# Optimization experiments

Measured on AMD Instinct MI355X. Metric: run time of the kernel, lower is better.

## Reference

```python
import jax, jax.numpy as jnp
import numpy as np


def batch_map_offsets(x, offsets):
    """Bilinear sampling of x at (pixel grid + offsets), coords clipped to borders.
    x: [B,H,W,C], offsets: [B,H,W,2] (dy, dx) in pixels. Returns [B,H,W,C]."""
    B, H, W, C = x.shape
    gy, gx = jnp.meshgrid(jnp.arange(H, dtype=x.dtype), jnp.arange(W, dtype=x.dtype), indexing='ij')
    cy = jnp.clip(gy[None] + offsets[..., 0], 0.0, H - 1)
    cx = jnp.clip(gx[None] + offsets[..., 1], 0.0, W - 1)
    y0 = jnp.floor(cy).astype(jnp.int32)
    x0 = jnp.floor(cx).astype(jnp.int32)
    y1 = jnp.clip(y0 + 1, 0, H - 1)
    x1 = jnp.clip(x0 + 1, 0, W - 1)
    wy = (cy - y0.astype(x.dtype))[..., None]
    wx = (cx - x0.astype(x.dtype))[..., None]
    b = jnp.arange(B)[:, None, None]
    g = lambda yi, xi: x[b, yi, xi]  # gather -> [B,H,W,C]
    top = g(y0, x0) * (1 - wx) + g(y0, x1) * wx
    bot = g(y1, x0) * (1 - wx) + g(y1, x1) * wx
    return top * (1 - wy) + bot * wy


def setup_inputs() -> dict:
    key = jax.random.key(0)
    k1, k2 = jax.random.split(key)
    B, H, W, C = 8, 256, 256, 64
    x = jax.random.normal(k1, (B, H, W, C), dtype=jnp.float32)
    reg = jax.random.normal(k2, (B, H, W, 4), dtype=jnp.float32)
    return {"x": x, "reg": reg, "frame": 8, "share": 1}


def reference(x, reg, frame, share):
    reg_in, reg_out = jnp.split(reg, 2, axis=3)
    x_reg = batch_map_offsets(x, reg_in)            # [B,H,W,C]
    B, H, W, C = x_reg.shape
    xr = x_reg.reshape(1, frame, H, W, C)
    x_max = jnp.max(xr, axis=1)                     # [1,H,W,C]
    x_mean = jnp.mean(xr, axis=1)                   # [1,H,W,C]
    xs = jnp.concatenate([x_max, x_mean], axis=3)   # [1,H,W,2C]
    # stack over frame then reshape back to batch (same shared features per frame)
    xs = jnp.broadcast_to(xs[:, None], (1, frame, H, W, 2 * C)).reshape(B, H, W, 2 * C)
    x_share_1 = batch_map_offsets(xs, reg_out)      # [B,H,W,2C]
    x_share_2 = jnp.concatenate([x, x], axis=3)     # [B,H,W,2C]
    return jnp.where(jnp.asarray(share) != 0, x_share_1, x_share_2)
```

## Files before the change

### kernel.cpp

```cpp
#include <hip/hip_runtime.h>


__global__ __launch_bounds__(256) void share_reduce_kernel(
    const float* __restrict__ x, const float* __restrict__ reg,
    float* __restrict__ xs)
{
    const int wid  = threadIdx.x >> 6;
    const int lane = threadIdx.x & 63;
    const int pix  = (blockIdx.x << 2) + wid;
    const int h = pix >> 8;
    const int w = pix & 255;

    float vmax = -INFINITY;
    float vsum = 0.f;

#pragma unroll
    for (int b = 0; b < 8; ++b) {
        const float* rp = reg + ((((b << 8) + h) << 8) + w) * 4;
        const float dy = rp[0];
        const float dx = rp[1];
        float cy = fminf(fmaxf((float)h + dy, 0.f), 255.f);
        float cx = fminf(fmaxf((float)w + dx, 0.f), 255.f);
        const float fy0 = floorf(cy);
        const float fx0 = floorf(cx);
        const int y0 = (int)fy0;
        const int x0 = (int)fx0;
        const int y1 = min(y0 + 1, 255);
        const int x1 = min(x0 + 1, 255);
        const float wy = cy - fy0;
        const float wx = cx - fx0;

        const float* xb = x + ((size_t)b << 22);
        const float v00 = xb[(((y0 << 8) + x0) << 6) + lane];
        const float v01 = xb[(((y0 << 8) + x1) << 6) + lane];
        const float v10 = xb[(((y1 << 8) + x0) << 6) + lane];
        const float v11 = xb[(((y1 << 8) + x1) << 6) + lane];

        const float top = v00 * (1.f - wx) + v01 * wx;
        const float bot = v10 * (1.f - wx) + v11 * wx;
        const float val = top * (1.f - wy) + bot * wy;

        vmax = fmaxf(vmax, val);
        vsum += val;
    }

    float* op = xs + ((size_t)pix << 7);
    op[lane]      = vmax;
    op[64 + lane] = vsum * 0.125f;
}

__global__ __launch_bounds__(256) void share_sample_kernel(
    const float* __restrict__ x, const float* __restrict__ reg,
    const float* __restrict__ xs, const int* __restrict__ share_p,
    float* __restrict__ out)
{
    const int wid  = threadIdx.x >> 6;
    const int lane = threadIdx.x & 63;
    const int pix  = (blockIdx.x << 2) + wid;
    const int hw = pix & 65535;
    const int h = hw >> 8;
    const int w = hw & 255;

    float* op = out + ((size_t)pix << 7);

    if (*share_p != 0) {
        const float* rp = reg + (size_t)pix * 4;
        const float dy = rp[2];
        const float dx = rp[3];
        float cy = fminf(fmaxf((float)h + dy, 0.f), 255.f);
        float cx = fminf(fmaxf((float)w + dx, 0.f), 255.f);
        const float fy0 = floorf(cy);
        const float fx0 = floorf(cx);
        const int y0 = (int)fy0;
        const int x0 = (int)fx0;
        const int y1 = min(y0 + 1, 255);
        const int x1 = min(x0 + 1, 255);
        const float wy = cy - fy0;
        const float wx = cx - fx0;

        const float2* r00 = (const float2*)(xs + ((size_t)(((y0 << 8) + x0)) << 7)) + lane;
        const float2* r01 = (const float2*)(xs + ((size_t)(((y0 << 8) + x1)) << 7)) + lane;
        const float2* r10 = (const float2*)(xs + ((size_t)(((y1 << 8) + x0)) << 7)) + lane;
        const float2* r11 = (const float2*)(xs + ((size_t)(((y1 << 8) + x1)) << 7)) + lane;
        const float2 v00 = *r00;
        const float2 v01 = *r01;
        const float2 v10 = *r10;
        const float2 v11 = *r11;

        float2 res;
        {
            const float top = v00.x * (1.f - wx) + v01.x * wx;
            const float bot = v10.x * (1.f - wx) + v11.x * wx;
            res.x = top * (1.f - wy) + bot * wy;
        }
        {
            const float top = v00.y * (1.f - wx) + v01.y * wx;
            const float bot = v10.y * (1.f - wx) + v11.y * wx;
            res.y = top * (1.f - wy) + bot * wy;
        }
        ((float2*)op)[lane] = res;
    } else {
        const float v = x[((size_t)pix << 6) + lane];
        op[lane]      = v;
        op[64 + lane] = v;
    }
}

extern "C" void kernel_launch(void* const* d_in, const int* in_sizes, int n_in,
                              void* d_out, int out_size, void* d_ws, size_t ws_size,
                              hipStream_t stream) {
    const float* x     = (const float*)d_in[0];
    const float* reg   = (const float*)d_in[1];
    const int*   share = (const int*)d_in[3];
    float* out = (float*)d_out;
    float* xs  = (float*)d_ws;

    share_reduce_kernel<<<65536 / 4, 256, 0, stream>>>(x, reg, xs);
    share_sample_kernel<<<524288 / 4, 256, 0, stream>>>(x, reg, xs, share, out);
}
```

Before: 471.1 us.

## Widen per-thread vector loads and swizzle block-to-pixel mapping in both kernels

Each wave now handles two pixels, with 32 lanes per pixel. The reduce kernel uses float2 loads and the sample kernel uses float4 loads and nontemporal float4 stores, so the grids shrink by half and by two. Block indices are interleaved so that adjacent hardware blocks work on spatially separated rows. The aim is fewer, wider memory instructions and less cache pollution from the large output write. The cost is different gather coalescing and a changed locality pattern from the swizzle.

```diff
diff --git a/kernel.cpp b/kernel.cpp
--- a/kernel.cpp
+++ b/kernel.cpp
@@ -1,26 +1,30 @@
 #include <hip/hip_runtime.h>
 
+
+typedef float f32x2 __attribute__((ext_vector_type(2)));
+typedef float f32x4 __attribute__((ext_vector_type(4)));
 
 __global__ __launch_bounds__(256) void share_reduce_kernel(
     const float* __restrict__ x, const float* __restrict__ reg,
     float* __restrict__ xs)
 {
-    const int wid  = threadIdx.x >> 6;
-    const int lane = threadIdx.x & 63;
-    const int pix  = (blockIdx.x << 2) + wid;
+    const int bid  = ((blockIdx.x & 7) << 10) + (blockIdx.x >> 3);
+    const int tid  = threadIdx.x;
+    const int half = (tid >> 5) & 1;
+    const int ln   = tid & 31;
+    const int pix  = (bid << 3) + ((tid >> 6) << 1) + half;
     const int h = pix >> 8;
     const int w = pix & 255;
+    const int c = ln << 1;
 
-    float vmax = -INFINITY;
-    float vsum = 0.f;
+    float m0 = -INFINITY, m1 = -INFINITY;
+    float s0 = 0.f, s1 = 0.f;
 
 #pragma unroll
     for (int b = 0; b < 8; ++b) {
-        const float* rp = reg + ((((b << 8) + h) << 8) + w) * 4;
-        const float dy = rp[0];
-        const float dx = rp[1];
-        float cy = fminf(fmaxf((float)h + dy, 0.f), 255.f);
-        float cx = fminf(fmaxf((float)w + dx, 0.f), 255.f);
+        const f32x2 r = *(const f32x2*)(reg + (size_t)((((b << 8) + h) << 8) + w) * 4);
+        float cy = fminf(fmaxf((float)h + r.x, 0.f), 255.f);
+        float cx = fminf(fmaxf((float)w + r.y, 0.f), 255.f);
         const float fy0 = floorf(cy);
         const float fx0 = floorf(cx);
         const int y0 = (int)fy0;
@@ -31,22 +35,29 @@
         const float wx = cx - fx0;
 
         const float* xb = x + ((size_t)b << 22);
-        const float v00 = xb[(((y0 << 8) + x0) << 6) + lane];
-        const float v01 = xb[(((y0 << 8) + x1) << 6) + lane];
-        const float v10 = xb[(((y1 << 8) + x0) << 6) + lane];
-        const float v11 = xb[(((y1 << 8) + x1) << 6) + lane];
+        const f32x2 v00 = *(const f32x2*)(xb + ((((y0 << 8) + x0) << 6) + c));
+        const f32x2 v01 = *(const f32x2*)(xb + ((((y0 << 8) + x1) << 6) + c));
+        const f32x2 v10 = *(const f32x2*)(xb + ((((y1 << 8) + x0) << 6) + c));
+        const f32x2 v11 = *(const f32x2*)(xb + ((((y1 << 8) + x1) << 6) + c));
 
-        const float top = v00 * (1.f - wx) + v01 * wx;
-        const float bot = v10 * (1.f - wx) + v11 * wx;
-        const float val = top * (1.f - wy) + bot * wy;
+        const float t0 = v00.x * (1.f - wx) + v01.x * wx;
+        const float t1 = v00.y * (1.f - wx) + v01.y * wx;
+        const float u0 = v10.x * (1.f - wx) + v11.x * wx;
+        const float u1 = v10.y * (1.f - wx) + v11.y * wx;
+        const float val0 = t0 * (1.f - wy) + u0 * wy;
+        const float val1 = t1 * (1.f - wy) + u1 * wy;
 
-        vmax = fmaxf(vmax, val);
-        vsum += val;
+        m0 = fmaxf(m0, val0);
+        m1 = fmaxf(m1, val1);
+        s0 += val0;
+        s1 += val1;
     }
 
     float* op = xs + ((size_t)pix << 7);
-    op[lane]      = vmax;
-    op[64 + lane] = vsum * 0.125f;
+    f32x2 vmax; vmax.x = m0; vmax.y = m1;
+    f32x2 vmean; vmean.x = s0 * 0.125f; vmean.y = s1 * 0.125f;
+    *(f32x2*)(op + c)      = vmax;
+    *(f32x2*)(op + 64 + c) = vmean;
 }
 
 __global__ __launch_bounds__(256) void share_sample_kernel(
@@ -54,21 +65,22 @@
     const float* __restrict__ xs, const int* __restrict__ share_p,
     float* __restrict__ out)
 {
-    const int wid  = threadIdx.x >> 6;
-    const int lane = threadIdx.x & 63;
-    const int pix  = (blockIdx.x << 2) + wid;
+    const int bid  = ((blockIdx.x & 7) << 13) + (blockIdx.x >> 3);
+    const int tid  = threadIdx.x;
+    const int half = (tid >> 5) & 1;
+    const int ln   = tid & 31;
+    const int pix  = (bid << 3) + ((tid >> 6) << 1) + half;
     const int hw = pix & 65535;
     const int h = hw >> 8;
     const int w = hw & 255;
+    const int c = ln << 2;
 
     float* op = out + ((size_t)pix << 7);
 
     if (*share_p != 0) {
-        const float* rp = reg + (size_t)pix * 4;
-        const float dy = rp[2];
-        const float dx = rp[3];
-        float cy = fminf(fmaxf((float)h + dy, 0.f), 255.f);
-        float cx = fminf(fmaxf((float)w + dx, 0.f), 255.f);
+        const f32x4 r = *(const f32x4*)(reg + (size_t)pix * 4);
+        float cy = fminf(fmaxf((float)h + r.z, 0.f), 255.f);
+        float cx = fminf(fmaxf((float)w + r.w, 0.f), 255.f);
         const float fy0 = floorf(cy);
         const float fx0 = floorf(cx);
         const int y0 = (int)fy0;
@@ -78,31 +90,18 @@
         const float wy = cy - fy0;
         const float wx = cx - fx0;
 
-        const float2* r00 = (const float2*)(xs + ((size_t)(((y0 << 8) + x0)) << 7)) + lane;
-        const float2* r01 = (const float2*)(xs + ((size_t)(((y0 << 8) + x1)) << 7)) + lane;
-        const float2* r10 = (const float2*)(xs + ((size_t)(((y1 << 8) + x0)) << 7)) + lane;
-        const float2* r11 = (const float2*)(xs + ((size_t)(((y1 << 8) + x1)) << 7)) + lane;
-        const float2 v00 = *r00;
-        const float2 v01 = *r01;
-        const float2 v10 = *r10;
-        const float2 v11 = *r11;
+        const f32x4 v00 = *(const f32x4*)(xs + (((size_t)((y0 << 8) + x0)) << 7) + c);
+        const f32x4 v01 = *(const f32x4*)(xs + (((size_t)((y0 << 8) + x1)) << 7) + c);
+        const f32x4 v10 = *(const f32x4*)(xs + (((size_t)((y1 << 8) + x0)) << 7) + c);
+        const f32x4 v11 = *(const f32x4*)(xs + (((size_t)((y1 << 8) + x1)) << 7) + c);
 
-        float2 res;
-        {
-            const float top = v00.x * (1.f - wx) + v01.x * wx;
-            const float bot = v10.x * (1.f - wx) + v11.x * wx;
-            res.x = top * (1.f - wy) + bot * wy;
-        }
-        {
-            const float top = v00.y * (1.f - wx) + v01.y * wx;
-            const float bot = v10.y * (1.f - wx) + v11.y * wx;
-            res.y = top * (1.f - wy) + bot * wy;
-        }
-        ((float2*)op)[lane] = res;
+        const f32x4 top = v00 * (1.f - wx) + v01 * wx;
+        const f32x4 bot = v10 * (1.f - wx) + v11 * wx;
+        const f32x4 res = top * (1.f - wy) + bot * wy;
+        __builtin_nontemporal_store(res, (f32x4*)(op + c));
     } else {
-        const float v = x[((size_t)pix << 6) + lane];
-        op[lane]      = v;
-        op[64 + lane] = v;
+        const f32x4 v = *(const f32x4*)(x + ((size_t)pix << 6) + (c & 63));
+        __builtin_nontemporal_store(v, (f32x4*)(op + c));
     }
 }
 
@@ -115,6 +114,6 @@
     float* out = (float*)d_out;
     float* xs  = (float*)d_ws;
 
-    share_reduce_kernel<<<65536 / 4, 256, 0, stream>>>(x, reg, xs);
-    share_sample_kernel<<<524288 / 4, 256, 0, stream>>>(x, reg, xs, share, out);
+    share_reduce_kernel<<<8192, 256, 0, stream>>>(x, reg, xs);
+    share_sample_kernel<<<65536, 256, 0, stream>>>(x, reg, xs, share, out);
 }
```

Measured after the change: 428.2 us. -9.1%, faster.
